# Optimization experiments

Hardware: AMD Instinct MI355X
Metric: run time of the kernel (lower is better)

The kernel has to match this reference:

```python
import jax, jax.numpy as jnp
import numpy as np

B, D, T = 8, 1024, 4096
Q, K, CD = 8, 1024, 32
COMMIT = 0.25
EPS = 1e-12


def setup_inputs() -> dict:
    key = jax.random.key(0)
    ks = jax.random.split(key, 6)
    x = jax.random.normal(ks[0], (B, D, T), dtype=jnp.float32)
    # stacked per-quantizer params: in_proj (1x1 conv == linear), out_proj, codebook
    Win = jax.random.normal(ks[1], (Q, CD, D), dtype=jnp.float32) * (1.0 / np.sqrt(D))
    b_in = jnp.zeros((Q, CD), dtype=jnp.float32)
    Wout = jax.random.normal(ks[2], (Q, D, CD), dtype=jnp.float32) * (1.0 / np.sqrt(CD))
    b_out = jnp.zeros((Q, D), dtype=jnp.float32)
    codebooks = jax.random.normal(ks[3], (Q, K, CD), dtype=jnp.float32)
    return {"x": x, "Win": Win, "b_in": b_in, "Wout": Wout, "b_out": b_out, "codebooks": codebooks}


def _l2norm(v):
    return v * jax.lax.rsqrt(jnp.sum(v * v, axis=-1, keepdims=True) + EPS)


def reference(x, Win, b_in, Wout, b_out, codebooks):
    """Residual VQ: sequential chain of factorized VQ layers.
    x: [B, D, T]. Returns (quantized_out [B,D,T], indices [Q,B,T], losses [Q]).
    """
    def step(residual, params):
        wi, bi, wo, bo, cb = params
        # in_proj: 1x1 conv == linear over channel dim
        z_e = jnp.einsum('bdt,cd->bct', residual, wi) + bi[None, :, None]  # [B,CD,T]
        enc = z_e.transpose(0, 2, 1).reshape(-1, z_e.shape[1])            # [B*T, CD]
        enc_n = _l2norm(enc)
        cb_n = _l2norm(cb)
        # full cdist^2 (argmin-equivalent, faithful to torch code)
        dist = (jnp.sum(enc_n * enc_n, -1, keepdims=True)
                - 2.0 * enc_n @ cb_n.T
                + jnp.sum(cb_n * cb_n, -1)[None, :])                       # [B*T, K]
        idx = jnp.argmin(dist, axis=-1).reshape(residual.shape[0], -1)     # [B, T]
        z_q = cb[idx].transpose(0, 2, 1)                                   # [B,CD,T]
        commit = jnp.mean((z_e - jax.lax.stop_gradient(z_q)) ** 2, axis=(1, 2))
        cbl = jnp.mean((z_q - jax.lax.stop_gradient(z_e)) ** 2, axis=(1, 2))
        loss = jnp.mean(COMMIT * commit + cbl)
        # straight-through estimator
        z_q = z_e + jax.lax.stop_gradient(z_q - z_e)
        q = jnp.einsum('bct,dc->bdt', z_q, wo) + bo[None, :, None]         # [B,D,T]
        return residual - q, (q, idx, loss)

    _, (qs, idxs, losses) = jax.lax.scan(step, x, (Win, b_in, Wout, b_out, codebooks))
    quantized_out = jnp.sum(qs, axis=0)
    return quantized_out, idxs, losses
```

## Files before the change

kernel.cpp:

```cpp
#include <hip/hip_runtime.h>
#include <math.h>

#define B 8
#define D 1024
#define T 4096
#define Q 8
#define K 1024
#define CD 32
#define BT (B * T)

#define OFF_Z0   ((size_t)0)
#define OFF_MT   (OFF_Z0 + (size_t)Q * B * CD * T * 8)
#define OFF_CBN  (OFF_MT + (size_t)64 * K * CD * 8)
#define OFF_N264 (OFF_CBN + (size_t)Q * K * CD * 8)
#define OFF_NT   (OFF_N264 + (size_t)Q * K * 8)
#define OFF_BEFF (OFF_NT + (size_t)64 * CD * CD * 8)
#define OFF_C32  (OFF_BEFF + (size_t)Q * CD * 8)
#define OFF_N232 (OFF_C32 + (size_t)Q * K * CD * 4)
#define OFF_W64  (OFF_N232 + (size_t)Q * K * 4)

typedef float f32x2 __attribute__((ext_vector_type(2)));

__device__ __forceinline__ f32x2 mk2(float a, float b) { f32x2 r; r.x = a; r.y = b; return r; }

__device__ __forceinline__ f32x2 pkfma(f32x2 a, f32x2 b, f32x2 c) {
    f32x2 d;
    asm("v_pk_fma_f32 %0, %1, %2, %3" : "=v"(d) : "v"(a), "v"(b), "v"(c));
    return d;
}

__global__ void k_zero_losses(float* __restrict__ loss) {
    if (threadIdx.x < Q) loss[threadIdx.x] = 0.0f;
}

__global__ __launch_bounds__(256) void k_norm(const float* __restrict__ cb,
                                              double* __restrict__ cbn64,
                                              double* __restrict__ n264,
                                              float* __restrict__ cbn32,
                                              float* __restrict__ n232) {
    int i = blockIdx.x * 256 + threadIdx.x;
    const float* c = cb + (size_t)i * CD;
    double v[CD];
    double ss = 0.0;
#pragma unroll
    for (int j = 0; j < CD; ++j) { v[j] = (double)c[j]; ss += v[j] * v[j]; }
    double s = 1.0 / sqrt(ss + 1e-12);
    double n2 = 0.0;
    double* o = cbn64 + (size_t)i * CD;
    float* o32 = cbn32 + (size_t)i * CD;
#pragma unroll
    for (int j = 0; j < CD; ++j) {
        double vn = v[j] * s;
        o[j] = vn; o32[j] = (float)vn; n2 += vn * vn;
    }
    n264[i] = n2; n232[i] = (float)n2;
}

__global__ __launch_bounds__(256) void k_cvtW(const float* __restrict__ Win,
                                              double* __restrict__ Win64) {
    int i = blockIdx.x * 256 + threadIdx.x;
    Win64[i] = (double)Win[i];
}

__global__ __launch_bounds__(256) void k_prep_N(const float* __restrict__ Win,
                                                const float* __restrict__ Wout,
                                                double* __restrict__ Ntab) {
    const int q = blockIdx.x >> 3, j = blockIdx.x & 7;
    __shared__ float a_sh[CD][128];
    __shared__ float b_sh[128][CD];
    double acc[4] = {0.0, 0.0, 0.0, 0.0};
    for (int d0 = 0; d0 < D; d0 += 128) {
        __syncthreads();
        for (int i = threadIdx.x; i < CD * 128; i += 256) {
            int cc = i >> 7, dl = i & 127;
            a_sh[cc][dl] = Win[((size_t)q * CD + cc) * D + d0 + dl];
        }
        for (int i = threadIdx.x; i < 128 * CD; i += 256) {
            int dl = i >> 5, cc = i & 31;
            b_sh[dl][cc] = Wout[((size_t)j * D + d0 + dl) * CD + cc];
        }
        __syncthreads();
        for (int dl = 0; dl < 128; ++dl) {
#pragma unroll
            for (int r = 0; r < 4; ++r) {
                int i = r * 256 + threadIdx.x;
                acc[r] = fma((double)a_sh[i >> 5][dl], (double)b_sh[dl][i & 31], acc[r]);
            }
        }
    }
#pragma unroll
    for (int r = 0; r < 4; ++r) {
        int i = r * 256 + threadIdx.x;
        Ntab[((size_t)(q * 8 + j) * CD + (i >> 5)) * CD + (i & 31)] = acc[r];
    }
}

__global__ __launch_bounds__(256) void k_prep_M(const float* __restrict__ cb,
                                                const double* __restrict__ Ntab,
                                                double* __restrict__ Mt) {
    const int q = blockIdx.z, j = blockIdx.y;
    const int k = blockIdx.x * 256 + threadIdx.x;
    __shared__ double nsh[CD][CD];
    for (int i = threadIdx.x; i < CD * CD; i += 256)
        nsh[i >> 5][i & 31] = Ntab[(size_t)(q * 8 + j) * CD * CD + i];
    __syncthreads();
    double cv[CD];
    const float* cr = cb + ((size_t)j * K + k) * CD;
#pragma unroll
    for (int c = 0; c < CD; ++c) cv[c] = (double)cr[c];
    double* mo = Mt + (((size_t)(q * 8 + j) * K + k) * CD);
#pragma unroll
    for (int c = 0; c < CD; ++c) {
        double a = 0.0;
#pragma unroll
        for (int cp = 0; cp < CD; ++cp) a = fma(nsh[c][cp], cv[cp], a);
        mo[c] = a;
    }
}

__global__ __launch_bounds__(256) void k_prep_beff(const float* __restrict__ Win,
                                                   const float* __restrict__ b_in,
                                                   const float* __restrict__ b_out,
                                                   double* __restrict__ beff) {
    const int c = blockIdx.x, q = blockIdx.y;
    __shared__ double red[256];
    double p = 0.0;
    for (int d = threadIdx.x; d < D; d += 256) {
        double bp = 0.0;
        for (int j = 0; j < q; ++j) bp += (double)b_out[j * D + d];
        p = fma((double)Win[((size_t)q * CD + c) * D + d], bp, p);
    }
    red[threadIdx.x] = p;
    __syncthreads();
    for (int s = 128; s > 0; s >>= 1) {
        if (threadIdx.x < s) red[threadIdx.x] += red[threadIdx.x + s];
        __syncthreads();
    }
    if (threadIdx.x == 0) beff[q * CD + c] = (double)b_in[q * CD + c] - red[0];
}

__global__ __launch_bounds__(256, 8) void k_gemmZ(const float* __restrict__ x,
                                                  const double* __restrict__ Win64,
                                                  const double* __restrict__ beff,
                                                  double* __restrict__ z0) {
    int h = blockIdx.x;
    int u = h >> 3, r = h & 7;
    int q = u & 7;
    int m = r + 8 * (u >> 3);
    int b = m >> 4;
    int tc = m & 15;
    int t = tc * 256 + threadIdx.x;
    const int c0 = blockIdx.y * (CD / 2);

    const double* w = Win64 + ((size_t)q * CD + c0) * D;
    const double* be = beff + q * CD + c0;
    const float* xb = x + (size_t)b * D * T + t;

    double acc[CD / 2];
#pragma unroll
    for (int c = 0; c < CD / 2; ++c) acc[c] = be[c];

    for (int d0 = 0; d0 < D; d0 += 8) {
        double xv[8];
#pragma unroll
        for (int i = 0; i < 8; ++i) xv[i] = (double)xb[(size_t)(d0 + i) * T];
#pragma unroll
        for (int c = 0; c < CD / 2; ++c) {
            const double* wc = w + (size_t)c * D + d0;
#pragma unroll
            for (int i = 0; i < 8; ++i) acc[c] = fma(wc[i], xv[i], acc[c]);
        }
    }
    double* zo = z0 + (((size_t)q * B + b) * CD + c0) * T + t;
#pragma unroll
    for (int c = 0; c < CD / 2; ++c) zo[(size_t)c * T] = acc[c];
}

#define INS4(dd, ii)                                                           \
    do {                                                                       \
        float _d = (dd); int _i = (ii);                                        \
        if (_d < d4) {                                                         \
            d4 = _d; i4 = _i;                                                  \
            if (d4 < d3) { float tf = d3; d3 = d4; d4 = tf; int ti = i3; i3 = i4; i4 = ti; } \
            if (d3 < d2) { float tf = d2; d2 = d3; d3 = tf; int ti = i2; i2 = i3; i3 = ti; } \
            if (d2 < d1) { float tf = d1; d1 = d2; d2 = tf; int ti = i1; i1 = i2; i2 = ti; } \
        }                                                                      \
    } while (0)

#define AT 64
__global__ __launch_bounds__(1024, 8) void k_argmin_fused(const double* __restrict__ z0,
                                                          const double* __restrict__ Mt,
                                                          const double* __restrict__ cbn64,
                                                          const double* __restrict__ n264,
                                                          const float* __restrict__ cbn32,
                                                          const float* __restrict__ n232,
                                                          const float* __restrict__ cb,
                                                          int* __restrict__ idxi,
                                                          float* __restrict__ idx_f,
                                                          float* __restrict__ loss) {
    const int lane = threadIdx.x & 63;
    const int wv = threadIdx.x >> 6;
    const int kcw = __builtin_amdgcn_readfirstlane(wv);
    const int t = blockIdx.x * AT + lane;
    const int b = blockIdx.y;
    const size_t bt = (size_t)b * T + t;

    __shared__ double zn_s[CD][AT];
    __shared__ f32x2  znf2_s[CD / 2][AT];
    __shared__ float  a2_s[AT];
    __shared__ double rn_s[AT];
    __shared__ float  sd[16][4][AT];
    __shared__ int    si[16][4][AT];
    __shared__ double ed[4][AT];
    __shared__ int    hist_s[Q][AT];

    for (int q = 0; q < Q; ++q) {
        {
            const int c0 = wv * 2;
            double v0 = z0[(((size_t)q * B + b) * CD + c0) * T + t];
            double v1 = z0[(((size_t)q * B + b) * CD + c0 + 1) * T + t];
            for (int j = 0; j < q; ++j) {
                int kj = hist_s[j][lane];
                const double* m = Mt + (((size_t)(q * 8 + j) * K + kj) * CD);
                v0 -= m[c0];
                v1 -= m[c0 + 1];
            }
            zn_s[c0][lane] = v0;
            zn_s[c0 + 1][lane] = v1;
        }
        __syncthreads();

        if (wv == 0) {
            double ss = 0.0;
#pragma unroll
            for (int c = 0; c < CD; ++c) { double v = zn_s[c][lane]; ss += v * v; }
            double rnorm = sqrt(ss + 1e-12);
            double s = 1.0 / rnorm;
            float a2 = 0.0f;
            float zf_prev = 0.0f;
#pragma unroll
            for (int c = 0; c < CD; ++c) {
                double vn = zn_s[c][lane] * s;
                zn_s[c][lane] = vn;
                float zf = (float)vn;
                a2 = fmaf(zf, zf, a2);
                if (c & 1) znf2_s[c >> 1][lane] = mk2(zf_prev, zf);
                else zf_prev = zf;
            }
            a2_s[lane] = a2;
            rn_s[lane] = rnorm;
        }
        __syncthreads();

        float d1 = 1e30f, d2 = 1e30f, d3 = 1e30f, d4 = 1e30f;
        int i1 = 0, i2 = 0, i3 = 0, i4 = 0;
        {
            const float a2v = a2_s[lane];
            const float4* cp = (const float4*)(cbn32 + ((size_t)q * K + (size_t)kcw * 64) * CD);
            const float* nq = n232 + q * K + kcw * 64;
            for (int k = 0; k < 64; k += 4) {
                const float4* c0 = cp + k * (CD / 4);
                f32x2 a0a = mk2(0.f, 0.f), a0b = mk2(0.f, 0.f);
                f32x2 a1a = mk2(0.f, 0.f), a1b = mk2(0.f, 0.f);
                f32x2 a2a = mk2(0.f, 0.f), a2b = mk2(0.f, 0.f);
                f32x2 a3a = mk2(0.f, 0.f), a3b = mk2(0.f, 0.f);
#pragma unroll
                for (int u = 0; u < CD / 4; ++u) {
                    f32x2 zpa = znf2_s[2 * u][lane];
                    f32x2 zpb = znf2_s[2 * u + 1][lane];
                    float4 av = c0[u];
                    float4 bv = c0[u + 8];
                    float4 cv = c0[u + 16];
                    float4 dv = c0[u + 24];
                    a0a = pkfma(zpa, mk2(av.x, av.y), a0a);
                    a0b = pkfma(zpb, mk2(av.z, av.w), a0b);
                    a1a = pkfma(zpa, mk2(bv.x, bv.y), a1a);
                    a1b = pkfma(zpb, mk2(bv.z, bv.w), a1b);
                    a2a = pkfma(zpa, mk2(cv.x, cv.y), a2a);
                    a2b = pkfma(zpb, mk2(cv.z, cv.w), a2b);
                    a3a = pkfma(zpa, mk2(dv.x, dv.y), a3a);
                    a3b = pkfma(zpb, mk2(dv.z, dv.w), a3b);
                }
                float dot0 = (a0a.x + a0b.x) + (a0a.y + a0b.y);
                float dot1 = (a1a.x + a1b.x) + (a1a.y + a1b.y);
                float dot2 = (a2a.x + a2b.x) + (a2a.y + a2b.y);
                float dot3 = (a3a.x + a3b.x) + (a3a.y + a3b.y);
                float dist0 = fmaf(-2.0f, dot0, a2v) + nq[k];
                float dist1 = fmaf(-2.0f, dot1, a2v) + nq[k + 1];
                float dist2 = fmaf(-2.0f, dot2, a2v) + nq[k + 2];
                float dist3 = fmaf(-2.0f, dot3, a2v) + nq[k + 3];
                INS4(dist0, kcw * 64 + k);
                INS4(dist1, kcw * 64 + k + 1);
                INS4(dist2, kcw * 64 + k + 2);
                INS4(dist3, kcw * 64 + k + 3);
            }
            sd[wv][0][lane] = d1; sd[wv][1][lane] = d2;
            sd[wv][2][lane] = d3; sd[wv][3][lane] = d4;
            si[wv][0][lane] = i1; si[wv][1][lane] = i2;
            si[wv][2][lane] = i3; si[wv][3][lane] = i4;
        }
        __syncthreads();

        if (wv < 4) {
            d1 = d2 = d3 = d4 = 1e30f; i1 = i2 = i3 = i4 = 0;
            for (int w = 0; w < 16; ++w)
#pragma unroll
                for (int s4 = 0; s4 < 4; ++s4)
                    INS4(sd[w][s4][lane], si[w][s4][lane]);

            if (d4 - d1 >= 1e-4f) {
                int j1 = i1, j2 = i2, j3 = i3, j4 = i4;
                { int tt; if (j1 > j2) { tt = j1; j1 = j2; j2 = tt; }
                          if (j3 > j4) { tt = j3; j3 = j4; j4 = tt; }
                          if (j1 > j3) { tt = j1; j1 = j3; j3 = tt; }
                          if (j2 > j4) { tt = j2; j2 = j4; j4 = tt; }
                          if (j2 > j3) { tt = j2; j2 = j3; j3 = tt; } }
                const int myj = (wv == 0) ? j1 : (wv == 1) ? j2 : (wv == 2) ? j3 : j4;
                const double* cp64 = cbn64 + ((size_t)q * K + myj) * CD;
                double A = 0.0, dot = 0.0;
#pragma unroll
                for (int c = 0; c < CD; ++c) {
                    double vn = zn_s[c][lane];
                    A += vn * vn;
                    dot = fma(vn, cp64[c], dot);
                }
                ed[wv][lane] = (A - 2.0 * dot) + n264[(size_t)q * K + myj];
            }
        }
        __syncthreads();

        if (wv == 0) {
            const double rnorm = rn_s[lane];
            int bi;
            if (d4 - d1 >= 1e-4f) {
                int j1 = i1, j2 = i2, j3 = i3, j4 = i4;
                { int tt; if (j1 > j2) { tt = j1; j1 = j2; j2 = tt; }
                          if (j3 > j4) { tt = j3; j3 = j4; j4 = tt; }
                          if (j1 > j3) { tt = j1; j1 = j3; j3 = tt; }
                          if (j2 > j4) { tt = j2; j2 = j4; j4 = tt; }
                          if (j2 > j3) { tt = j2; j2 = j3; j3 = tt; } }
                double e1 = ed[0][lane], e2 = ed[1][lane];
                double e3 = ed[2][lane], e4 = ed[3][lane];
                double best = e1; bi = j1;
                if (e2 < best) { best = e2; bi = j2; }
                if (e3 < best) { best = e3; bi = j3; }
                if (e4 < best) { best = e4; bi = j4; }
            } else {
                double zn[CD]; double A = 0.0;
#pragma unroll
                for (int c = 0; c < CD; ++c) { zn[c] = zn_s[c][lane]; A += zn[c] * zn[c]; }
                double best = 1e300; bi = 0;
                const double* cq64 = cbn64 + (size_t)q * K * CD;
                const double* nq64 = n264 + (size_t)q * K;
                for (int k = 0; k < K; k += 2) {
                    double dot0 = 0.0, dot1 = 0.0;
                    const double* c0 = cq64 + (size_t)k * CD;
                    const double* c1 = c0 + CD;
#pragma unroll
                    for (int c = 0; c < CD; ++c) {
                        dot0 = fma(zn[c], c0[c], dot0);
                        dot1 = fma(zn[c], c1[c], dot1);
                    }
                    double dist0 = (A - 2.0 * dot0) + nq64[k];
                    double dist1 = (A - 2.0 * dot1) + nq64[k + 1];
                    if (dist0 < best) { best = dist0; bi = k; }
                    if (dist1 < best) { best = dist1; bi = k + 1; }
                }
            }
            hist_s[q][lane] = bi;

            const float* cr = cb + ((size_t)q * K + bi) * CD;
            double sq = 0.0;
#pragma unroll
            for (int c = 0; c < CD; ++c) {
                double diff = zn_s[c][lane] * rnorm - (double)cr[c];
                sq = fma(diff, diff, sq);
            }
#pragma unroll
            for (int off = 32; off > 0; off >>= 1) sq += __shfl_down(sq, off);
            if (lane == 0)
                atomicAdd(&loss[q], (float)(sq * (1.25 / (double)((size_t)B * CD * T))));
            idxi[q * BT + bt] = bi;
            idx_f[(size_t)q * BT + bt] = (float)bi;
        }
        __syncthreads();
    }
}

#define GT 128
#define GD 128
__global__ __launch_bounds__(256) void k_gemm_final(const float* __restrict__ Wout,
                                                    const float* __restrict__ bo,
                                                    const float* __restrict__ cb,
                                                    const int* __restrict__ idxi,
                                                    float* __restrict__ out) {
    const int t0 = blockIdx.x * GT;
    const int b  = blockIdx.y;
    const int d0 = blockIdx.z * GD;
    const int tx = threadIdx.x & 15;
    const int ty = threadIdx.x >> 4;
    __shared__ float Wt[CD][GD + 4];
    __shared__ float Zt[CD][GT + 4];
    __shared__ float bsum[GD];

    if (threadIdx.x < GD) {
        float sjb = 0.0f;
#pragma unroll
        for (int j = 0; j < Q; ++j) sjb += bo[j * D + d0 + threadIdx.x];
        bsum[threadIdx.x] = sjb;
    }

    float acc[8][8];
#pragma unroll
    for (int r = 0; r < 8; ++r)
#pragma unroll
        for (int cc = 0; cc < 8; ++cc) acc[r][cc] = 0.0f;

    for (int j = 0; j < Q; ++j) {
        __syncthreads();
        for (int i = threadIdx.x; i < GD * CD; i += 256) {
            int dl = i >> 5, c = i & 31;
            Wt[c][dl] = Wout[((size_t)j * D + d0 + dl) * CD + c];
        }
        for (int i = threadIdx.x; i < GT * CD; i += 256) {
            int tl = i >> 5, c = i & 31;
            int kj = idxi[j * BT + (size_t)b * T + t0 + tl];
            Zt[c][tl] = cb[((size_t)j * K + kj) * CD + c];
        }
        __syncthreads();
#pragma unroll
        for (int k = 0; k < CD; ++k) {
            float a[8], zb[8];
            *(float4*)&a[0]  = *(const float4*)&Wt[k][ty * 8];
            *(float4*)&a[4]  = *(const float4*)&Wt[k][ty * 8 + 4];
            *(float4*)&zb[0] = *(const float4*)&Zt[k][tx * 8];
            *(float4*)&zb[4] = *(const float4*)&Zt[k][tx * 8 + 4];
#pragma unroll
            for (int r = 0; r < 8; ++r)
#pragma unroll
                for (int cc = 0; cc < 8; ++cc)
                    acc[r][cc] = fmaf(a[r], zb[cc], acc[r][cc]);
        }
    }
#pragma unroll
    for (int r = 0; r < 8; ++r) {
        const int d = d0 + ty * 8 + r;
        const float bias = bsum[ty * 8 + r];
        float4 v0, v1;
        v0.x = acc[r][0] + bias; v0.y = acc[r][1] + bias;
        v0.z = acc[r][2] + bias; v0.w = acc[r][3] + bias;
        v1.x = acc[r][4] + bias; v1.y = acc[r][5] + bias;
        v1.z = acc[r][6] + bias; v1.w = acc[r][7] + bias;
        float* op = out + ((size_t)b * D + d) * T + t0 + tx * 8;
        *(float4*)op = v0;
        *(float4*)(op + 4) = v1;
    }
}

extern "C" void kernel_launch(void* const* d_in, const int* in_sizes, int n_in,
                              void* d_out, int out_size, void* d_ws, size_t ws_size,
                              hipStream_t stream) {
    const float* x     = (const float*)d_in[0];
    const float* Win   = (const float*)d_in[1];
    const float* b_in  = (const float*)d_in[2];
    const float* Wout  = (const float*)d_in[3];
    const float* b_out = (const float*)d_in[4];
    const float* cb    = (const float*)d_in[5];

    float* out0  = (float*)d_out;
    float* idx_f = out0 + (size_t)B * D * T;
    float* loss  = idx_f + (size_t)Q * BT;

    char* sc = (char*)d_out;
    double* z0    = (double*)(sc + OFF_Z0);
    double* Mt    = (double*)(sc + OFF_MT);
    double* cbn64 = (double*)(sc + OFF_CBN);
    double* n264  = (double*)(sc + OFF_N264);
    double* Ntab  = (double*)(sc + OFF_NT);
    double* beff  = (double*)(sc + OFF_BEFF);
    float*  cbn32 = (float*)(sc + OFF_C32);
    float*  n232  = (float*)(sc + OFF_N232);
    double* Win64 = (double*)(sc + OFF_W64);
    int*    idxi  = (int*)d_ws;

    k_zero_losses<<<1, 64, 0, stream>>>(loss);
    k_norm<<<(Q * K) / 256, 256, 0, stream>>>(cb, cbn64, n264, cbn32, n232);
    k_cvtW<<<(Q * CD * D) / 256, 256, 0, stream>>>(Win, Win64);
    k_prep_N<<<64, 256, 0, stream>>>(Win, Wout, Ntab);
    k_prep_M<<<dim3(K / 256, 8, 8), 256, 0, stream>>>(cb, Ntab, Mt);
    k_prep_beff<<<dim3(CD, Q), 256, 0, stream>>>(Win, b_in, b_out, beff);

    k_gemmZ<<<dim3(Q * B * (T / 256), 2), 256, 0, stream>>>(x, Win64, beff, z0);

    k_argmin_fused<<<dim3(T / AT, B), 1024, 0, stream>>>(z0, Mt, cbn64, n264,
                                                         cbn32, n232, cb,
                                                         idxi, idx_f, loss);

    k_gemm_final<<<dim3(T / GT, B, D / GD), 256, 0, stream>>>(Wout, b_out, cb, idxi, out0);
}
```

Before: 1.479 ms.

## Compute per-wave normalization redundantly, drop barrier and skip fp64 refine when margin clear

Every wave now computes the residual's norm and its fp32 normalized copy in registers, instead of wave 0 doing it and publishing through shared memory behind an extra __syncthreads. The packed-FMA dot products over shared-memory operands become scalar FMAs over register operands. The fp64 refinement of the top-4 candidates is skipped when the best fp32 distance beats the second best by at least 1e-4, so that case takes index i1 directly. In exchange the normalization work is repeated in all 16 waves, register pressure rises, and the clear-margin shortcut relies on fp32 accuracy.

```diff
diff --git a/kernel.cpp b/kernel.cpp
--- a/kernel.cpp
+++ b/kernel.cpp
@@ -18,16 +18,6 @@
 #define OFF_C32  (OFF_BEFF + (size_t)Q * CD * 8)
 #define OFF_N232 (OFF_C32 + (size_t)Q * K * CD * 4)
 #define OFF_W64  (OFF_N232 + (size_t)Q * K * 4)
-
-typedef float f32x2 __attribute__((ext_vector_type(2)));
-
-__device__ __forceinline__ f32x2 mk2(float a, float b) { f32x2 r; r.x = a; r.y = b; return r; }
-
-__device__ __forceinline__ f32x2 pkfma(f32x2 a, f32x2 b, f32x2 c) {
-    f32x2 d;
-    asm("v_pk_fma_f32 %0, %1, %2, %3" : "=v"(d) : "v"(a), "v"(b), "v"(c));
-    return d;
-}
 
 __global__ void k_zero_losses(float* __restrict__ loss) {
     if (threadIdx.x < Q) loss[threadIdx.x] = 0.0f;
@@ -206,9 +196,6 @@
     const size_t bt = (size_t)b * T + t;
 
     __shared__ double zn_s[CD][AT];
-    __shared__ f32x2  znf2_s[CD / 2][AT];
-    __shared__ float  a2_s[AT];
-    __shared__ double rn_s[AT];
     __shared__ float  sd[16][4][AT];
     __shared__ int    si[16][4][AT];
     __shared__ double ed[4][AT];
@@ -230,65 +217,54 @@
         }
         __syncthreads();
 
-        if (wv == 0) {
-            double ss = 0.0;
-#pragma unroll
-            for (int c = 0; c < CD; ++c) { double v = zn_s[c][lane]; ss += v * v; }
-            double rnorm = sqrt(ss + 1e-12);
-            double s = 1.0 / rnorm;
-            float a2 = 0.0f;
-            float zf_prev = 0.0f;
-#pragma unroll
-            for (int c = 0; c < CD; ++c) {
-                double vn = zn_s[c][lane] * s;
-                zn_s[c][lane] = vn;
-                float zf = (float)vn;
-                a2 = fmaf(zf, zf, a2);
-                if (c & 1) znf2_s[c >> 1][lane] = mk2(zf_prev, zf);
-                else zf_prev = zf;
-            }
-            a2_s[lane] = a2;
-            rn_s[lane] = rnorm;
-        }
-        __syncthreads();
-
+        double s, rnorm;
         float d1 = 1e30f, d2 = 1e30f, d3 = 1e30f, d4 = 1e30f;
         int i1 = 0, i2 = 0, i3 = 0, i4 = 0;
         {
-            const float a2v = a2_s[lane];
+            double ss = 0.0;
+#pragma unroll
+            for (int c = 0; c < CD; ++c) { double v = zn_s[c][lane]; ss += v * v; }
+            rnorm = sqrt(ss + 1e-12);
+            s = 1.0 / rnorm;
+            float znf[CD];
+            float a2 = 0.0f;
+#pragma unroll
+            for (int c = 0; c < CD; ++c) {
+                double vn = zn_s[c][lane] * s;
+                float zf = (float)vn;
+                znf[c] = zf;
+                a2 = fmaf(zf, zf, a2);
+            }
+
             const float4* cp = (const float4*)(cbn32 + ((size_t)q * K + (size_t)kcw * 64) * CD);
             const float* nq = n232 + q * K + kcw * 64;
             for (int k = 0; k < 64; k += 4) {
                 const float4* c0 = cp + k * (CD / 4);
-                f32x2 a0a = mk2(0.f, 0.f), a0b = mk2(0.f, 0.f);
-                f32x2 a1a = mk2(0.f, 0.f), a1b = mk2(0.f, 0.f);
-                f32x2 a2a = mk2(0.f, 0.f), a2b = mk2(0.f, 0.f);
-                f32x2 a3a = mk2(0.f, 0.f), a3b = mk2(0.f, 0.f);
+                float p0 = 0.f, p1 = 0.f, p2 = 0.f, p3 = 0.f;
+                float r0 = 0.f, r1 = 0.f, r2 = 0.f, r3 = 0.f;
+                float s0 = 0.f, s1 = 0.f, s2 = 0.f, s3 = 0.f;
+                float u0 = 0.f, u1 = 0.f, u2 = 0.f, u3 = 0.f;
 #pragma unroll
                 for (int u = 0; u < CD / 4; ++u) {
-                    f32x2 zpa = znf2_s[2 * u][lane];
-                    f32x2 zpb = znf2_s[2 * u + 1][lane];
                     float4 av = c0[u];
                     float4 bv = c0[u + 8];
                     float4 cv = c0[u + 16];
                     float4 dv = c0[u + 24];
-                    a0a = pkfma(zpa, mk2(av.x, av.y), a0a);
-                    a0b = pkfma(zpb, mk2(av.z, av.w), a0b);
-                    a1a = pkfma(zpa, mk2(bv.x, bv.y), a1a);
-                    a1b = pkfma(zpb, mk2(bv.z, bv.w), a1b);
-                    a2a = pkfma(zpa, mk2(cv.x, cv.y), a2a);
-                    a2b = pkfma(zpb, mk2(cv.z, cv.w), a2b);
-                    a3a = pkfma(zpa, mk2(dv.x, dv.y), a3a);
-                    a3b = pkfma(zpb, mk2(dv.z, dv.w), a3b);
+                    float z0f = znf[u * 4 + 0], z1f = znf[u * 4 + 1];
+                    float z2f = znf[u * 4 + 2], z3f = znf[u * 4 + 3];
+                    p0 = fmaf(z0f, av.x, p0); p1 = fmaf(z1f, av.y, p1);
+                    p2 = fmaf(z2f, av.z, p2); p3 = fmaf(z3f, av.w, p3);
+                    r0 = fmaf(z0f, bv.x, r0); r1 = fmaf(z1f, bv.y, r1);
+                    r2 = fmaf(z2f, bv.z, r2); r3 = fmaf(z3f, bv.w, r3);
+                    s0 = fmaf(z0f, cv.x, s0); s1 = fmaf(z1f, cv.y, s1);
+                    s2 = fmaf(z2f, cv.z, s2); s3 = fmaf(z3f, cv.w, s3);
+                    u0 = fmaf(z0f, dv.x, u0); u1 = fmaf(z1f, dv.y, u1);
+                    u2 = fmaf(z2f, dv.z, u2); u3 = fmaf(z3f, dv.w, u3);
                 }
-                float dot0 = (a0a.x + a0b.x) + (a0a.y + a0b.y);
-                float dot1 = (a1a.x + a1b.x) + (a1a.y + a1b.y);
-                float dot2 = (a2a.x + a2b.x) + (a2a.y + a2b.y);
-                float dot3 = (a3a.x + a3b.x) + (a3a.y + a3b.y);
-                float dist0 = fmaf(-2.0f, dot0, a2v) + nq[k];
-                float dist1 = fmaf(-2.0f, dot1, a2v) + nq[k + 1];
-                float dist2 = fmaf(-2.0f, dot2, a2v) + nq[k + 2];
-                float dist3 = fmaf(-2.0f, dot3, a2v) + nq[k + 3];
+                float dist0 = fmaf(-2.0f, (p0 + p1) + (p2 + p3), a2) + nq[k];
+                float dist1 = fmaf(-2.0f, (r0 + r1) + (r2 + r3), a2) + nq[k + 1];
+                float dist2 = fmaf(-2.0f, (s0 + s1) + (s2 + s3), a2) + nq[k + 2];
+                float dist3 = fmaf(-2.0f, (u0 + u1) + (u2 + u3), a2) + nq[k + 3];
                 INS4(dist0, kcw * 64 + k);
                 INS4(dist1, kcw * 64 + k + 1);
                 INS4(dist2, kcw * 64 + k + 2);
@@ -308,7 +284,7 @@
                 for (int s4 = 0; s4 < 4; ++s4)
                     INS4(sd[w][s4][lane], si[w][s4][lane]);
 
-            if (d4 - d1 >= 1e-4f) {
+            if (d2 - d1 < 1e-4f && d4 - d1 >= 1e-4f) {
                 int j1 = i1, j2 = i2, j3 = i3, j4 = i4;
                 { int tt; if (j1 > j2) { tt = j1; j1 = j2; j2 = tt; }
                           if (j3 > j4) { tt = j3; j3 = j4; j4 = tt; }
@@ -320,7 +296,7 @@
                 double A = 0.0, dot = 0.0;
 #pragma unroll
                 for (int c = 0; c < CD; ++c) {
-                    double vn = zn_s[c][lane];
+                    double vn = zn_s[c][lane] * s;
                     A += vn * vn;
                     dot = fma(vn, cp64[c], dot);
                 }
@@ -330,9 +306,10 @@
         __syncthreads();
 
         if (wv == 0) {
-            const double rnorm = rn_s[lane];
             int bi;
-            if (d4 - d1 >= 1e-4f) {
+            if (d2 - d1 >= 1e-4f) {
+                bi = i1;
+            } else if (d4 - d1 >= 1e-4f) {
                 int j1 = i1, j2 = i2, j3 = i3, j4 = i4;
                 { int tt; if (j1 > j2) { tt = j1; j1 = j2; j2 = tt; }
                           if (j3 > j4) { tt = j3; j3 = j4; j4 = tt; }
@@ -348,7 +325,10 @@
             } else {
                 double zn[CD]; double A = 0.0;
 #pragma unroll
-                for (int c = 0; c < CD; ++c) { zn[c] = zn_s[c][lane]; A += zn[c] * zn[c]; }
+                for (int c = 0; c < CD; ++c) {
+                    zn[c] = zn_s[c][lane] * s;
+                    A += zn[c] * zn[c];
+                }
                 double best = 1e300; bi = 0;
                 const double* cq64 = cbn64 + (size_t)q * K * CD;
                 const double* nq64 = n264 + (size_t)q * K;
@@ -373,7 +353,8 @@
             double sq = 0.0;
 #pragma unroll
             for (int c = 0; c < CD; ++c) {
-                double diff = zn_s[c][lane] * rnorm - (double)cr[c];
+                double vn = zn_s[c][lane] * s;
+                double diff = vn * rnorm - (double)cr[c];
                 sq = fma(diff, diff, sq);
             }
 #pragma unroll
```

Result: slower. 1.569 ms (+6.1%).
